# Kernel optimization log

Measured on AMD Instinct MI355X. Metric: run time of the kernel, lower is better.

## Reference

```python
import jax, jax.numpy as jnp
import numpy as np

KS = 9          # ms_ks in the original module
PAD = KS // 2   # conv padding along H
B, C, H, W = 32, 1, 384, 1280


def _corr_h(col, w):
    """9-tap cross-correlation along H with zero padding.
    col: [B, H], w: [KS] -> [B, H]. Matches torch Conv2d(1,1,(9,1),padding=(4,0))
    applied to a [B,1,H,1] column."""
    p = jnp.pad(col, ((0, 0), (PAD, PAD)))
    acc = w[0] * p[:, 0:H]
    for k in range(1, KS):  # static unroll over the 9 taps
        acc = acc + w[k] * p[:, k:k + H]
    return acc


def _scan_pass(xs, w, reverse):
    """Sequential message passing over columns.
    xs: [W, B, H]; out[i] = xs[i] + relu(corr(out[i-1], w)), out[0] = xs[0]."""
    if reverse:
        xs = xs[::-1]

    def step(carry, xcol):
        new = xcol + jax.nn.relu(_corr_h(carry, w))
        return new, new

    _, outs = jax.lax.scan(step, xs[0], xs[1:])
    out = jnp.concatenate([xs[:1], outs], axis=0)
    if reverse:
        out = out[::-1]
    return out


def setup_inputs() -> dict:
    key = jax.random.key(0)
    k1, k2, k3 = jax.random.split(key, 3)
    x = jax.random.uniform(k1, (B, C, H, W), dtype=jnp.float32)  # sigmoid disparity in [0,1]
    bound = 1.0 / np.sqrt(KS)  # torch Conv2d default init bound (fan_in = 1*9*1)
    w_lr = jax.random.uniform(k2, (KS,), dtype=jnp.float32, minval=-bound, maxval=bound)
    w_rl = jax.random.uniform(k3, (KS,), dtype=jnp.float32, minval=-bound, maxval=bound)
    return {"x": x, "w_lr": w_lr, "w_rl": w_rl}


def reference(x, w_lr, w_rl):
    # x: [B, 1, H, W] -> columns-first [W, B, H]
    xs = jnp.transpose(x[:, 0], (2, 0, 1))
    xs = _scan_pass(xs, w_lr, reverse=False)  # left -> right
    xs = _scan_pass(xs, w_rl, reverse=True)   # right -> left
    return jnp.transpose(xs, (1, 2, 0))[:, None, :, :]  # [B, 1, H, W]
```

## Files before the change

kernel.cpp:

```cpp
#include <hip/hip_runtime.h>

#define BB 32
#define HH 384
#define WW 1280
#define KS 9
#define NL 64

typedef float f2v __attribute__((ext_vector_type(2)));
typedef float4 f4;

__device__ __forceinline__ float dpp_up1(float v) {
    return __int_as_float(__builtin_amdgcn_mov_dpp(__float_as_int(v), 0x138, 0xf, 0xf, true));
}
__device__ __forceinline__ float dpp_dn1(float v) {
    return __int_as_float(__builtin_amdgcn_mov_dpp(__float_as_int(v), 0x130, 0xf, 0xf, true));
}
__device__ __forceinline__ float comp4(const f4& q, int u) {
    return (u == 0) ? q.x : (u == 1) ? q.y : (u == 2) ? q.z : q.w;
}
__device__ __forceinline__ void set4(f4& q, int u, float val) {
    if (u == 0) q.x = val; else if (u == 1) q.y = val;
    else if (u == 2) q.z = val; else q.w = val;
}

__device__ __forceinline__ void conv9h(const f2v (&V)[3], const f2v (&Wp)[KS],
                                       const float (&w)[KS], f2v (&A)[3]) {
    f2v P0, P1, P5, P6;
    P0.x = dpp_up1(V[1].x); P0.y = dpp_up1(V[1].y);
    P1.x = dpp_up1(V[2].x); P1.y = dpp_up1(V[2].y);
    P5.x = dpp_dn1(V[0].x); P5.y = dpp_dn1(V[0].y);
    P6.x = dpp_dn1(V[1].x); P6.y = dpp_dn1(V[1].y);
    const f2v P[7] = {P0, P1, V[0], V[1], V[2], P5, P6};
#pragma unroll
    for (int p = 0; p < 3; ++p) {
        f2v a = Wp[0] * P[p];
        a = __builtin_elementwise_fma(Wp[2], P[p + 1], a);
        a = __builtin_elementwise_fma(Wp[4], P[p + 2], a);
        a = __builtin_elementwise_fma(Wp[6], P[p + 3], a);
        a = __builtin_elementwise_fma(Wp[8], P[p + 4], a);
        float ax = a.x, ay = a.y;
        ax = fmaf(w[1], P[p].y,     ax);
        ax = fmaf(w[3], P[p + 1].y, ax);
        ax = fmaf(w[5], P[p + 2].y, ax);
        ax = fmaf(w[7], P[p + 3].y, ax);
        ay = fmaf(w[1], P[p + 1].x, ay);
        ay = fmaf(w[3], P[p + 2].x, ay);
        ay = fmaf(w[5], P[p + 3].x, ay);
        ay = fmaf(w[7], P[p + 4].x, ay);
        A[p].x = fmaxf(ax, 0.f);
        A[p].y = fmaxf(ay, 0.f);
    }
}

__device__ __forceinline__ void ldx(const float* __restrict__ xb, int h0, int col,
                                    f4 (&X)[6]) {
#pragma unroll
    for (int j = 0; j < 6; ++j)
        X[j] = *(const f4*)(xb + (size_t)(h0 + j) * WW + col);
}

template<bool FIRST>
__device__ __forceinline__ void p1g(f2v (&V)[3], const f4 (&X)[6],
                                    const f2v (&Wp)[KS], const float (&w)[KS],
                                    f2v* __restrict__ wsb, int l, int w0) {
#pragma unroll
    for (int u = 0; u < 4; ++u) {
        if (FIRST && u == 0) {
            V[0].x = X[0].x; V[0].y = X[1].x;
            V[1].x = X[2].x; V[1].y = X[3].x;
            V[2].x = X[4].x; V[2].y = X[5].x;
        } else {
            f2v A[3];
            conv9h(V, Wp, w, A);
            V[0].x = comp4(X[0], u) + A[0].x;  V[0].y = comp4(X[1], u) + A[0].y;
            V[1].x = comp4(X[2], u) + A[1].x;  V[1].y = comp4(X[3], u) + A[1].y;
            V[2].x = comp4(X[4], u) + A[2].x;  V[2].y = comp4(X[5], u) + A[2].y;
        }
        f2v* c = wsb + (size_t)(w0 + u) * 192;
        c[l] = V[0]; c[l + 64] = V[1]; c[l + 128] = V[2];
    }
}

__device__ __forceinline__ void ldo(const f2v* __restrict__ wsb, int l, int w0,
                                    f2v (&OG)[4][3]) {
#pragma unroll
    for (int u = 0; u < 4; ++u) {
        const f2v* c = wsb + (size_t)(w0 + u) * 192;
        OG[u][0] = c[l]; OG[u][1] = c[l + 64]; OG[u][2] = c[l + 128];
    }
}

template<bool FIRST>
__device__ __forceinline__ void p2g(f2v (&V)[3], const f2v (&OG)[4][3], int cbase,
                                    f4 (&ob)[6][2], const f2v (&Wp)[KS],
                                    const float (&w)[KS]) {
#pragma unroll
    for (int uu = 0; uu < 4; ++uu) {
        const int u = 3 - uu;
        if (FIRST && u == 3) {
            V[0] = OG[3][0]; V[1] = OG[3][1]; V[2] = OG[3][2];
        } else {
            f2v A[3];
            conv9h(V, Wp, w, A);
            V[0] = OG[u][0] + A[0];
            V[1] = OG[u][1] + A[1];
            V[2] = OG[u][2] + A[2];
        }
        const int c = cbase + u;
        set4(ob[0][c >> 2], c & 3, V[0].x);
        set4(ob[1][c >> 2], c & 3, V[0].y);
        set4(ob[2][c >> 2], c & 3, V[1].x);
        set4(ob[3][c >> 2], c & 3, V[1].y);
        set4(ob[4][c >> 2], c & 3, V[2].x);
        set4(ob[5][c >> 2], c & 3, V[2].y);
    }
}

__device__ __forceinline__ void flush8(const f4 (&ob)[6][2], float* __restrict__ outb,
                                       int h0, int w8) {
#pragma unroll
    for (int j = 0; j < 6; ++j) {
        *(f4*)(outb + (size_t)(h0 + j) * WW + w8)     = ob[j][0];
        *(f4*)(outb + (size_t)(h0 + j) * WW + w8 + 4) = ob[j][1];
    }
}

__global__ __launch_bounds__(NL, 1) void scnn_scan(const float* __restrict__ x,
                                                   float* __restrict__ ws,
                                                   float* __restrict__ out,
                                                   const float* __restrict__ w_lr,
                                                   const float* __restrict__ w_rl) {
    const int b  = blockIdx.x;
    const int l  = threadIdx.x;
    const int h0 = l * 6;

    const float* xb   = x   + (size_t)b * HH * WW;
    float*       outb = out + (size_t)b * HH * WW;
    f2v*         wsb  = (f2v*)ws + (size_t)b * WW * 192;

    float wl[KS], wr[KS];
    f2v Wlp[KS], Wrp[KS];
#pragma unroll
    for (int k = 0; k < KS; ++k) {
        wl[k] = w_lr[k]; wr[k] = w_rl[k];
        f2v ta, tc;
        ta.x = wl[k]; ta.y = wl[k];  tc.x = wr[k]; tc.y = wr[k];
        Wlp[k] = ta; Wrp[k] = tc;
    }

    f2v V[3];

    {
        f4 XA[6], XB[6], XC[6], XD[6];
        ldx(xb, h0, 0, XA); ldx(xb, h0, 4, XB); ldx(xb, h0, 8, XC); ldx(xb, h0, 12, XD);
        p1g<true >(V, XA, Wlp, wl, wsb, l, 0);  ldx(xb, h0, 16, XA);
        p1g<false>(V, XB, Wlp, wl, wsb, l, 4);  ldx(xb, h0, 20, XB);
        p1g<false>(V, XC, Wlp, wl, wsb, l, 8);  ldx(xb, h0, 24, XC);
        p1g<false>(V, XD, Wlp, wl, wsb, l, 12); ldx(xb, h0, 28, XD);
#pragma unroll 1
        for (int m = 1; m < 79; ++m) {
            const int c0 = 16 * m;
            p1g<false>(V, XA, Wlp, wl, wsb, l, c0 + 0);  ldx(xb, h0, c0 + 16, XA);
            p1g<false>(V, XB, Wlp, wl, wsb, l, c0 + 4);  ldx(xb, h0, c0 + 20, XB);
            p1g<false>(V, XC, Wlp, wl, wsb, l, c0 + 8);  ldx(xb, h0, c0 + 24, XC);
            p1g<false>(V, XD, Wlp, wl, wsb, l, c0 + 12); ldx(xb, h0, c0 + 28, XD);
        }
        p1g<false>(V, XA, Wlp, wl, wsb, l, 1264);
        p1g<false>(V, XB, Wlp, wl, wsb, l, 1268);
        p1g<false>(V, XC, Wlp, wl, wsb, l, 1272);
        p1g<false>(V, XD, Wlp, wl, wsb, l, 1276);
    }

    asm volatile("s_waitcnt vmcnt(0)" ::: "memory");

    {
        f2v GA[4][3], GB[4][3], GC[4][3], GD[4][3];
        ldo(wsb, l, 1276, GA);
        ldo(wsb, l, 1272, GB);
        ldo(wsb, l, 1268, GC);
        ldo(wsb, l, 1264, GD);
        f4 ob[6][2];
        p2g<true >(V, GA, 4, ob, Wrp, wr); ldo(wsb, l, 1260, GA);
        p2g<false>(V, GB, 0, ob, Wrp, wr); ldo(wsb, l, 1256, GB);
        flush8(ob, outb, h0, 1272);
        p2g<false>(V, GC, 4, ob, Wrp, wr); ldo(wsb, l, 1252, GC);
        p2g<false>(V, GD, 0, ob, Wrp, wr); ldo(wsb, l, 1248, GD);
        flush8(ob, outb, h0, 1264);
#pragma unroll 1
        for (int t = 1; t < 79; ++t) {
            const int cA = 1276 - 16 * t;
            p2g<false>(V, GA, 4, ob, Wrp, wr); ldo(wsb, l, cA - 16, GA);
            p2g<false>(V, GB, 0, ob, Wrp, wr); ldo(wsb, l, cA - 20, GB);
            flush8(ob, outb, h0, cA - 4);
            p2g<false>(V, GC, 4, ob, Wrp, wr); ldo(wsb, l, cA - 24, GC);
            p2g<false>(V, GD, 0, ob, Wrp, wr); ldo(wsb, l, cA - 28, GD);
            flush8(ob, outb, h0, cA - 12);
        }
        p2g<false>(V, GA, 4, ob, Wrp, wr);
        p2g<false>(V, GB, 0, ob, Wrp, wr);
        flush8(ob, outb, h0, 8);
        p2g<false>(V, GC, 4, ob, Wrp, wr);
        p2g<false>(V, GD, 0, ob, Wrp, wr);
        flush8(ob, outb, h0, 0);
    }
}

extern "C" void kernel_launch(void* const* d_in, const int* in_sizes, int n_in,
                              void* d_out, int out_size, void* d_ws, size_t ws_size,
                              hipStream_t stream) {
    const float* x    = (const float*)d_in[0];
    const float* w_lr = (const float*)d_in[1];
    const float* w_rl = (const float*)d_in[2];
    float* out = (float*)d_out;
    float* ws  = (float*)d_ws;

    scnn_scan<<<BB, NL, 0, stream>>>(x, ws, out, w_lr, w_rl);
}
```

Before: 401.4 us.

## Pre-transpose input into column-pair layout and scan it in place

Result: faster. 343.3 us (-14.5%).

```diff
diff --git a/kernel.cpp b/kernel.cpp
--- a/kernel.cpp
+++ b/kernel.cpp
@@ -5,9 +5,11 @@
 #define WW 1280
 #define KS 9
 #define NL 64
+#define NP 640
+#define BSTRIDE (NP * 192)
 
 typedef float f2v __attribute__((ext_vector_type(2)));
-typedef float4 f4;
+typedef float f4v __attribute__((ext_vector_type(4)));
 
 __device__ __forceinline__ float dpp_up1(float v) {
     return __int_as_float(__builtin_amdgcn_mov_dpp(__float_as_int(v), 0x138, 0xf, 0xf, true));
@@ -15,22 +17,55 @@
 __device__ __forceinline__ float dpp_dn1(float v) {
     return __int_as_float(__builtin_amdgcn_mov_dpp(__float_as_int(v), 0x130, 0xf, 0xf, true));
 }
-__device__ __forceinline__ float comp4(const f4& q, int u) {
-    return (u == 0) ? q.x : (u == 1) ? q.y : (u == 2) ? q.z : q.w;
-}
-__device__ __forceinline__ void set4(f4& q, int u, float val) {
+__device__ __forceinline__ void set4(f4v& q, int u, float val) {
     if (u == 0) q.x = val; else if (u == 1) q.y = val;
     else if (u == 2) q.z = val; else q.w = val;
 }
 
-__device__ __forceinline__ void conv9h(const f2v (&V)[3], const f2v (&Wp)[KS],
-                                       const float (&w)[KS], f2v (&A)[3]) {
+__global__ __launch_bounds__(512) void scnn_tr(const float* __restrict__ x,
+                                               f4v* __restrict__ xp) {
+    __shared__ float tile[HH][33];
+    const int b  = blockIdx.y;
+    const int c0 = blockIdx.x * 32;
+    const int t  = threadIdx.x;
+    const int col = t & 31;
+    const int r0  = t >> 5;
+    const float* xb = x + (size_t)b * HH * WW + c0;
+#pragma unroll
+    for (int k = 0; k < 24; ++k) {
+        const int r = r0 + 16 * k;
+        tile[r][col] = xb[(size_t)r * WW + col];
+    }
+    __syncthreads();
+    f4v* xpb = xp + (size_t)b * BSTRIDE + (size_t)(c0 >> 1) * 192;
+#pragma unroll
+    for (int i = 0; i < 6; ++i) {
+        const int idx = i * 512 + t;
+        const int qq  = idx / 192;
+        const int rem = idx - qq * 192;
+        const int p   = rem >> 6;
+        const int l   = rem & 63;
+        const int h   = 6 * l + 2 * p;
+        const int cc  = 2 * qq;
+        f4v v;
+        v.x = tile[h][cc];     v.y = tile[h + 1][cc];
+        v.z = tile[h][cc + 1]; v.w = tile[h + 1][cc + 1];
+        xpb[idx] = v;
+    }
+}
+
+template<bool ZW>
+__device__ __forceinline__ void conv9(const f4v (&VV)[3], const f2v (&Wp)[KS],
+                                      const float (&w)[KS], f2v (&A)[3]) {
+    f2v V0, V1, V2;
+    if constexpr (ZW) { V0 = VV[0].zw; V1 = VV[1].zw; V2 = VV[2].zw; }
+    else              { V0 = VV[0].xy; V1 = VV[1].xy; V2 = VV[2].xy; }
     f2v P0, P1, P5, P6;
-    P0.x = dpp_up1(V[1].x); P0.y = dpp_up1(V[1].y);
-    P1.x = dpp_up1(V[2].x); P1.y = dpp_up1(V[2].y);
-    P5.x = dpp_dn1(V[0].x); P5.y = dpp_dn1(V[0].y);
-    P6.x = dpp_dn1(V[1].x); P6.y = dpp_dn1(V[1].y);
-    const f2v P[7] = {P0, P1, V[0], V[1], V[2], P5, P6};
+    P0.x = dpp_up1(V1.x); P0.y = dpp_up1(V1.y);
+    P1.x = dpp_up1(V2.x); P1.y = dpp_up1(V2.y);
+    P5.x = dpp_dn1(V0.x); P5.y = dpp_dn1(V0.y);
+    P6.x = dpp_dn1(V1.x); P6.y = dpp_dn1(V1.y);
+    const f2v P[7] = {P0, P1, V0, V1, V2, P5, P6};
 #pragma unroll
     for (int p = 0; p < 3; ++p) {
         f2v a = Wp[0] * P[p];
@@ -52,81 +87,97 @@
     }
 }
 
-__device__ __forceinline__ void ldx(const float* __restrict__ xb, int h0, int col,
-                                    f4 (&X)[6]) {
-#pragma unroll
-    for (int j = 0; j < 6; ++j)
-        X[j] = *(const f4*)(xb + (size_t)(h0 + j) * WW + col);
-}
-
-template<bool FIRST>
-__device__ __forceinline__ void p1g(f2v (&V)[3], const f4 (&X)[6],
-                                    const f2v (&Wp)[KS], const float (&w)[KS],
-                                    f2v* __restrict__ wsb, int l, int w0) {
-#pragma unroll
-    for (int u = 0; u < 4; ++u) {
-        if (FIRST && u == 0) {
-            V[0].x = X[0].x; V[0].y = X[1].x;
-            V[1].x = X[2].x; V[1].y = X[3].x;
-            V[2].x = X[4].x; V[2].y = X[5].x;
-        } else {
-            f2v A[3];
-            conv9h(V, Wp, w, A);
-            V[0].x = comp4(X[0], u) + A[0].x;  V[0].y = comp4(X[1], u) + A[0].y;
-            V[1].x = comp4(X[2], u) + A[1].x;  V[1].y = comp4(X[3], u) + A[1].y;
-            V[2].x = comp4(X[4], u) + A[2].x;  V[2].y = comp4(X[5], u) + A[2].y;
-        }
-        f2v* c = wsb + (size_t)(w0 + u) * 192;
-        c[l] = V[0]; c[l + 64] = V[1]; c[l + 128] = V[2];
-    }
-}
-
-__device__ __forceinline__ void ldo(const f2v* __restrict__ wsb, int l, int w0,
-                                    f2v (&OG)[4][3]) {
-#pragma unroll
-    for (int u = 0; u < 4; ++u) {
-        const f2v* c = wsb + (size_t)(w0 + u) * 192;
-        OG[u][0] = c[l]; OG[u][1] = c[l + 64]; OG[u][2] = c[l + 128];
-    }
-}
-
-template<bool FIRST>
-__device__ __forceinline__ void p2g(f2v (&V)[3], const f2v (&OG)[4][3], int cbase,
-                                    f4 (&ob)[6][2], const f2v (&Wp)[KS],
-                                    const float (&w)[KS]) {
-#pragma unroll
-    for (int uu = 0; uu < 4; ++uu) {
-        const int u = 3 - uu;
-        if (FIRST && u == 3) {
-            V[0] = OG[3][0]; V[1] = OG[3][1]; V[2] = OG[3][2];
-        } else {
-            f2v A[3];
-            conv9h(V, Wp, w, A);
-            V[0] = OG[u][0] + A[0];
-            V[1] = OG[u][1] + A[1];
-            V[2] = OG[u][2] + A[2];
-        }
-        const int c = cbase + u;
-        set4(ob[0][c >> 2], c & 3, V[0].x);
-        set4(ob[1][c >> 2], c & 3, V[0].y);
-        set4(ob[2][c >> 2], c & 3, V[1].x);
-        set4(ob[3][c >> 2], c & 3, V[1].y);
-        set4(ob[4][c >> 2], c & 3, V[2].x);
-        set4(ob[5][c >> 2], c & 3, V[2].y);
-    }
-}
-
-__device__ __forceinline__ void flush8(const f4 (&ob)[6][2], float* __restrict__ outb,
+__device__ __forceinline__ void ldxp(const f4v* __restrict__ wsb, int l, int pq,
+                                     f4v (&X)[2][3]) {
+    const f4v* c = wsb + (size_t)pq * 192 + l;
+    X[0][0] = c[0];   X[0][1] = c[64];  X[0][2] = c[128];
+    X[1][0] = c[192]; X[1][1] = c[256]; X[1][2] = c[320];
+}
+
+template<bool FIRST>
+__device__ __forceinline__ void p1pair(f4v (&VV)[3], const f4v (&XP)[3],
+                                       const f2v (&Wp)[KS], const float (&w)[KS],
+                                       f4v* __restrict__ cbase, int l) {
+    if (FIRST) {
+        VV[0].xy = XP[0].xy; VV[1].xy = XP[1].xy; VV[2].xy = XP[2].xy;
+    } else {
+        f2v A[3];
+        conv9<true>(VV, Wp, w, A);
+        VV[0].xy = XP[0].xy + A[0];
+        VV[1].xy = XP[1].xy + A[1];
+        VV[2].xy = XP[2].xy + A[2];
+    }
+    {
+        f2v A[3];
+        conv9<false>(VV, Wp, w, A);
+        VV[0].zw = XP[0].zw + A[0];
+        VV[1].zw = XP[1].zw + A[1];
+        VV[2].zw = XP[2].zw + A[2];
+    }
+    cbase[l] = VV[0]; cbase[l + 64] = VV[1]; cbase[l + 128] = VV[2];
+}
+
+template<bool FIRST>
+__device__ __forceinline__ void p1grp(f4v (&VV)[3], const f4v (&X)[2][3],
+                                      f4v* __restrict__ wsb, int pq, int l,
+                                      const f2v (&Wp)[KS], const float (&w)[KS]) {
+    p1pair<FIRST>(VV, X[0], Wp, w, wsb + (size_t)pq * 192, l);
+    p1pair<false>(VV, X[1], Wp, w, wsb + (size_t)(pq + 1) * 192, l);
+}
+
+template<bool FIRST>
+__device__ __forceinline__ void p2pair(f4v (&VV)[3], const f4v (&OG)[3],
+                                       f4v (&ob)[6][2], int chi,
+                                       const f2v (&Wp)[KS], const float (&w)[KS]) {
+    if (FIRST) {
+        VV[0].zw = OG[0].zw; VV[1].zw = OG[1].zw; VV[2].zw = OG[2].zw;
+    } else {
+        f2v A[3];
+        conv9<false>(VV, Wp, w, A);
+        VV[0].zw = OG[0].zw + A[0];
+        VV[1].zw = OG[1].zw + A[1];
+        VV[2].zw = OG[2].zw + A[2];
+    }
+    set4(ob[0][chi >> 2], chi & 3, VV[0].z);
+    set4(ob[1][chi >> 2], chi & 3, VV[0].w);
+    set4(ob[2][chi >> 2], chi & 3, VV[1].z);
+    set4(ob[3][chi >> 2], chi & 3, VV[1].w);
+    set4(ob[4][chi >> 2], chi & 3, VV[2].z);
+    set4(ob[5][chi >> 2], chi & 3, VV[2].w);
+    {
+        f2v A[3];
+        conv9<true>(VV, Wp, w, A);
+        VV[0].xy = OG[0].xy + A[0];
+        VV[1].xy = OG[1].xy + A[1];
+        VV[2].xy = OG[2].xy + A[2];
+    }
+    const int clo = chi - 1;
+    set4(ob[0][clo >> 2], clo & 3, VV[0].x);
+    set4(ob[1][clo >> 2], clo & 3, VV[0].y);
+    set4(ob[2][clo >> 2], clo & 3, VV[1].x);
+    set4(ob[3][clo >> 2], clo & 3, VV[1].y);
+    set4(ob[4][clo >> 2], clo & 3, VV[2].x);
+    set4(ob[5][clo >> 2], clo & 3, VV[2].y);
+}
+
+template<bool FIRST>
+__device__ __forceinline__ void p2grp(f4v (&VV)[3], const f4v (&G)[2][3],
+                                      f4v (&ob)[6][2], int cbase,
+                                      const f2v (&Wp)[KS], const float (&w)[KS]) {
+    p2pair<FIRST>(VV, G[1], ob, cbase + 3, Wp, w);
+    p2pair<false>(VV, G[0], ob, cbase + 1, Wp, w);
+}
+
+__device__ __forceinline__ void flush8(const f4v (&ob)[6][2], float* __restrict__ outb,
                                        int h0, int w8) {
 #pragma unroll
     for (int j = 0; j < 6; ++j) {
-        *(f4*)(outb + (size_t)(h0 + j) * WW + w8)     = ob[j][0];
-        *(f4*)(outb + (size_t)(h0 + j) * WW + w8 + 4) = ob[j][1];
-    }
-}
-
-__global__ __launch_bounds__(NL, 1) void scnn_scan(const float* __restrict__ x,
-                                                   float* __restrict__ ws,
+        *(f4v*)(outb + (size_t)(h0 + j) * WW + w8)     = ob[j][0];
+        *(f4v*)(outb + (size_t)(h0 + j) * WW + w8 + 4) = ob[j][1];
+    }
+}
+
+__global__ __launch_bounds__(NL, 1) void scnn_scan(f4v* __restrict__ xp,
                                                    float* __restrict__ out,
                                                    const float* __restrict__ w_lr,
                                                    const float* __restrict__ w_rl) {
@@ -134,9 +185,8 @@
     const int l  = threadIdx.x;
     const int h0 = l * 6;
 
-    const float* xb   = x   + (size_t)b * HH * WW;
-    float*       outb = out + (size_t)b * HH * WW;
-    f2v*         wsb  = (f2v*)ws + (size_t)b * WW * 192;
+    f4v*   wsb  = xp  + (size_t)b * BSTRIDE;
+    float* outb = out + (size_t)b * HH * WW;
 
     float wl[KS], wr[KS];
     f2v Wlp[KS], Wrp[KS];
@@ -148,59 +198,57 @@
         Wlp[k] = ta; Wrp[k] = tc;
     }
 
-    f2v V[3];
-
-    {
-        f4 XA[6], XB[6], XC[6], XD[6];
-        ldx(xb, h0, 0, XA); ldx(xb, h0, 4, XB); ldx(xb, h0, 8, XC); ldx(xb, h0, 12, XD);
-        p1g<true >(V, XA, Wlp, wl, wsb, l, 0);  ldx(xb, h0, 16, XA);
-        p1g<false>(V, XB, Wlp, wl, wsb, l, 4);  ldx(xb, h0, 20, XB);
-        p1g<false>(V, XC, Wlp, wl, wsb, l, 8);  ldx(xb, h0, 24, XC);
-        p1g<false>(V, XD, Wlp, wl, wsb, l, 12); ldx(xb, h0, 28, XD);
+    f4v VV[3];
+
+    {
+        f4v XA[2][3], XB[2][3], XC[2][3], XD[2][3];
+        ldxp(wsb, l, 0, XA); ldxp(wsb, l, 2, XB); ldxp(wsb, l, 4, XC); ldxp(wsb, l, 6, XD);
+        p1grp<true >(VV, XA, wsb, 0, l, Wlp, wl); ldxp(wsb, l, 8,  XA);
+        p1grp<false>(VV, XB, wsb, 2, l, Wlp, wl); ldxp(wsb, l, 10, XB);
+        p1grp<false>(VV, XC, wsb, 4, l, Wlp, wl); ldxp(wsb, l, 12, XC);
+        p1grp<false>(VV, XD, wsb, 6, l, Wlp, wl); ldxp(wsb, l, 14, XD);
 #pragma unroll 1
         for (int m = 1; m < 79; ++m) {
-            const int c0 = 16 * m;
-            p1g<false>(V, XA, Wlp, wl, wsb, l, c0 + 0);  ldx(xb, h0, c0 + 16, XA);
-            p1g<false>(V, XB, Wlp, wl, wsb, l, c0 + 4);  ldx(xb, h0, c0 + 20, XB);
-            p1g<false>(V, XC, Wlp, wl, wsb, l, c0 + 8);  ldx(xb, h0, c0 + 24, XC);
-            p1g<false>(V, XD, Wlp, wl, wsb, l, c0 + 12); ldx(xb, h0, c0 + 28, XD);
+            const int pq0 = 8 * m;
+            p1grp<false>(VV, XA, wsb, pq0 + 0, l, Wlp, wl); ldxp(wsb, l, pq0 + 8,  XA);
+            p1grp<false>(VV, XB, wsb, pq0 + 2, l, Wlp, wl); ldxp(wsb, l, pq0 + 10, XB);
+            p1grp<false>(VV, XC, wsb, pq0 + 4, l, Wlp, wl); ldxp(wsb, l, pq0 + 12, XC);
+            p1grp<false>(VV, XD, wsb, pq0 + 6, l, Wlp, wl); ldxp(wsb, l, pq0 + 14, XD);
         }
-        p1g<false>(V, XA, Wlp, wl, wsb, l, 1264);
-        p1g<false>(V, XB, Wlp, wl, wsb, l, 1268);
-        p1g<false>(V, XC, Wlp, wl, wsb, l, 1272);
-        p1g<false>(V, XD, Wlp, wl, wsb, l, 1276);
+        p1grp<false>(VV, XA, wsb, 632, l, Wlp, wl);
+        p1grp<false>(VV, XB, wsb, 634, l, Wlp, wl);
+        p1grp<false>(VV, XC, wsb, 636, l, Wlp, wl);
+        p1grp<false>(VV, XD, wsb, 638, l, Wlp, wl);
     }
 
     asm volatile("s_waitcnt vmcnt(0)" ::: "memory");
 
     {
-        f2v GA[4][3], GB[4][3], GC[4][3], GD[4][3];
-        ldo(wsb, l, 1276, GA);
-        ldo(wsb, l, 1272, GB);
-        ldo(wsb, l, 1268, GC);
-        ldo(wsb, l, 1264, GD);
-        f4 ob[6][2];
-        p2g<true >(V, GA, 4, ob, Wrp, wr); ldo(wsb, l, 1260, GA);
-        p2g<false>(V, GB, 0, ob, Wrp, wr); ldo(wsb, l, 1256, GB);
+        f4v GA[2][3], GB[2][3], GC[2][3], GD[2][3];
+        ldxp(wsb, l, 638, GA); ldxp(wsb, l, 636, GB);
+        ldxp(wsb, l, 634, GC); ldxp(wsb, l, 632, GD);
+        f4v ob[6][2];
+        p2grp<true >(VV, GA, ob, 4, Wrp, wr); ldxp(wsb, l, 630, GA);
+        p2grp<false>(VV, GB, ob, 0, Wrp, wr); ldxp(wsb, l, 628, GB);
         flush8(ob, outb, h0, 1272);
-        p2g<false>(V, GC, 4, ob, Wrp, wr); ldo(wsb, l, 1252, GC);
-        p2g<false>(V, GD, 0, ob, Wrp, wr); ldo(wsb, l, 1248, GD);
+        p2grp<false>(VV, GC, ob, 4, Wrp, wr); ldxp(wsb, l, 626, GC);
+        p2grp<false>(VV, GD, ob, 0, Wrp, wr); ldxp(wsb, l, 624, GD);
         flush8(ob, outb, h0, 1264);
 #pragma unroll 1
-        for (int t = 1; t < 79; ++t) {
-            const int cA = 1276 - 16 * t;
-            p2g<false>(V, GA, 4, ob, Wrp, wr); ldo(wsb, l, cA - 16, GA);
-            p2g<false>(V, GB, 0, ob, Wrp, wr); ldo(wsb, l, cA - 20, GB);
-            flush8(ob, outb, h0, cA - 4);
-            p2g<false>(V, GC, 4, ob, Wrp, wr); ldo(wsb, l, cA - 24, GC);
-            p2g<false>(V, GD, 0, ob, Wrp, wr); ldo(wsb, l, cA - 28, GD);
-            flush8(ob, outb, h0, cA - 12);
+        for (int t2 = 1; t2 < 79; ++t2) {
+            const int pqA = 638 - 8 * t2;
+            p2grp<false>(VV, GA, ob, 4, Wrp, wr); ldxp(wsb, l, pqA - 8,  GA);
+            p2grp<false>(VV, GB, ob, 0, Wrp, wr); ldxp(wsb, l, pqA - 10, GB);
+            flush8(ob, outb, h0, 2 * pqA - 4);
+            p2grp<false>(VV, GC, ob, 4, Wrp, wr); ldxp(wsb, l, pqA - 12, GC);
+            p2grp<false>(VV, GD, ob, 0, Wrp, wr); ldxp(wsb, l, pqA - 14, GD);
+            flush8(ob, outb, h0, 2 * pqA - 12);
         }
-        p2g<false>(V, GA, 4, ob, Wrp, wr);
-        p2g<false>(V, GB, 0, ob, Wrp, wr);
+        p2grp<false>(VV, GA, ob, 4, Wrp, wr);
+        p2grp<false>(VV, GB, ob, 0, Wrp, wr);
         flush8(ob, outb, h0, 8);
-        p2g<false>(V, GC, 4, ob, Wrp, wr);
-        p2g<false>(V, GD, 0, ob, Wrp, wr);
+        p2grp<false>(VV, GC, ob, 4, Wrp, wr);
+        p2grp<false>(VV, GD, ob, 0, Wrp, wr);
         flush8(ob, outb, h0, 0);
     }
 }
@@ -212,7 +260,8 @@
     const float* w_lr = (const float*)d_in[1];
     const float* w_rl = (const float*)d_in[2];
     float* out = (float*)d_out;
-    float* ws  = (float*)d_ws;
-
-    scnn_scan<<<BB, NL, 0, stream>>>(x, ws, out, w_lr, w_rl);
-}
+    f4v*   xp  = (f4v*)d_ws;
+
+    scnn_tr<<<dim3(WW / 32, BB), 512, 0, stream>>>(x, xp);
+    scnn_scan<<<BB, NL, 0, stream>>>(xp, out, w_lr, w_rl);
+}
```
